# Kernel optimization log

Measured on AMD Instinct MI355X. Metric: run time of the kernel, lower is better.

The kernel has to match this reference:

```python
import jax, jax.numpy as jnp
import numpy as np

B, N, E = 128, 196, 2048   # batch, num_features (14x14), encoder_dim
D, A = 512, 512            # decoder_dim, attention_dim


def setup_inputs() -> dict:
    key = jax.random.key(0)
    ks = jax.random.split(key, 8)
    s_e = 1.0 / np.sqrt(E)
    s_d = 1.0 / np.sqrt(D)
    s_a = 1.0 / np.sqrt(A)
    return {
        "encoder_out": jax.random.normal(ks[0], (B, N, E), dtype=jnp.float32),
        "decoder_hidden": jax.random.normal(ks[1], (B, D), dtype=jnp.float32),
        "We": jax.random.uniform(ks[2], (E, A), jnp.float32, -s_e, s_e),
        "be": jax.random.uniform(ks[3], (A,), jnp.float32, -s_e, s_e),
        "Wd": jax.random.uniform(ks[4], (D, A), jnp.float32, -s_d, s_d),
        "bd": jax.random.uniform(ks[5], (A,), jnp.float32, -s_d, s_d),
        "Wf": jax.random.uniform(ks[6], (A, 1), jnp.float32, -s_a, s_a),
        "bf": jax.random.uniform(ks[7], (1,), jnp.float32, -s_a, s_a),
    }


def reference(encoder_out, decoder_hidden, We, be, Wd, bd, Wf, bf):
    # att1: [B,N,A] projection of encoder features
    att1 = jnp.einsum('bne,ea->bna', encoder_out, We) + be
    # att2: [B,A] projection of decoder state, broadcast over N
    att2 = decoder_hidden @ Wd + bd
    att = jnp.tanh(att1 + att2[:, None, :])          # [B,N,A]
    scores = jnp.einsum('bna,ao->bno', att, Wf) + bf  # [B,N,1]
    alpha = jax.nn.softmax(scores, axis=1)            # softmax over num_features
    context = jnp.sum(encoder_out * alpha, axis=1)    # [B,E]
    return (context, alpha)
```

## Files before the change

### kernel.cpp

```cpp
#include <hip/hip_runtime.h>
#include <hip/hip_bf16.h>
#include <stdint.h>

#define B_   128
#define N_   196
#define E_   2048
#define D_   512
#define A_   512
#define MTOT (B_ * N_)

typedef short  short8  __attribute__((ext_vector_type(8)));
typedef float  floatx4 __attribute__((ext_vector_type(4)));

__device__ __forceinline__ unsigned short f2bf(float f) {
    union { float f; uint32_t u; } v; v.f = f;
    uint32_t r = v.u + 0x7FFFu + ((v.u >> 16) & 1u);
    return (unsigned short)(r >> 16);
}

__global__ void transcvt_k(const float* __restrict__ We, unsigned short* __restrict__ WeT) {
    __shared__ float tile[32][33];
    const int e0 = blockIdx.x * 32, a0 = blockIdx.y * 32;
    const int t = threadIdx.x, tc = t & 31, tr = t >> 5;
#pragma unroll
    for (int i = 0; i < 4; ++i) {
        int r = tr + i * 8;
        tile[r][tc] = We[(size_t)(e0 + r) * A_ + a0 + tc];
    }
    __syncthreads();
#pragma unroll
    for (int i = 0; i < 4; ++i) {
        int r = tr + i * 8;
        WeT[(size_t)(a0 + r) * E_ + e0 + tc] = f2bf(tile[tc][r]);
    }
}

__launch_bounds__(512)
__global__ void att2_k(const float* __restrict__ dh, const float* __restrict__ Wd,
                       const float* __restrict__ bd, const float* __restrict__ be,
                       float* __restrict__ att2p) {
    const int b = blockIdx.x, t = threadIdx.x;
    __shared__ float sdh[D_];
    sdh[t] = dh[b * D_ + t];
    __syncthreads();
    float acc = 0.f;
#pragma unroll 8
    for (int d = 0; d < D_; ++d) acc += sdh[d] * Wd[(size_t)d * A_ + t];
    att2p[(size_t)b * A_ + t] = acc + bd[t] + be[t];
}

__launch_bounds__(256, 3)
__global__ void score_gemm(const float* __restrict__ enc,
                           const unsigned short* __restrict__ WeT,
                           const float* __restrict__ att2p,
                           const float* __restrict__ Wf,
                           float* __restrict__ scoresP) {
    __shared__ __align__(16) unsigned short sA[64 * 40];
    __shared__ __align__(16) unsigned short sB[256 * 32];
    __shared__ float sPart[4][64];

    const int t   = threadIdx.x;
    const int w   = t >> 6;
    const int l   = t & 63;
    const int l15 = l & 15;
    const int q4  = l >> 4;
    const int row0 = blockIdx.y * 64;
    const int cw0  = blockIdx.x * 256;

    floatx4 acc[4][4] = {};

    const int idx1 = t + 256;
    const int ar0 = t >> 3,    ac0 = (t & 7) * 4;
    const int ar1 = idx1 >> 3, ac1 = (idx1 & 7) * 4;
    const float* encA0 = enc + (size_t)(row0 + ar0) * E_ + ac0;
    const float* encA1 = enc + (size_t)(row0 + ar1) * E_ + ac1;

    const unsigned short* bsrc[4];
    int bdst[4];
#pragma unroll
    for (int j = 0; j < 4; ++j) {
        int s    = (w * 4 + j) * 64 + l;
        int nloc = s >> 2;
        int q    = (s & 3) ^ ((nloc >> 2) & 3);
        bsrc[j]  = WeT + (size_t)(cw0 + nloc) * E_ + q * 8;
        bdst[j]  = (w * 4 + j) * 1024;
    }

    for (int k0 = 0; k0 < E_; k0 += 32) {
#pragma unroll
        for (int j = 0; j < 4; ++j) {
            __builtin_amdgcn_global_load_lds(
                (const __attribute__((address_space(1))) uint32_t*)(bsrc[j] + k0),
                (__attribute__((address_space(3))) uint32_t*)((char*)sB + bdst[j]),
                16, 0, 0);
        }
        float4 v0 = *(const float4*)(encA0 + k0);
        float4 v1 = *(const float4*)(encA1 + k0);
        ushort4 h0 = { f2bf(v0.x), f2bf(v0.y), f2bf(v0.z), f2bf(v0.w) };
        ushort4 h1 = { f2bf(v1.x), f2bf(v1.y), f2bf(v1.z), f2bf(v1.w) };
        *(ushort4*)&sA[ar0 * 40 + ac0] = h0;
        *(ushort4*)&sA[ar1 * 40 + ac1] = h1;
        __syncthreads();

        short8 af[4], bfr[4];
#pragma unroll
        for (int mi = 0; mi < 4; ++mi)
            af[mi] = *(const short8*)&sA[(mi * 16 + l15) * 40 + q4 * 8];
#pragma unroll
        for (int ni = 0; ni < 4; ++ni) {
            int nloc = w * 64 + ni * 16 + l15;
            int slot = nloc * 4 + (q4 ^ ((nloc >> 2) & 3));
            bfr[ni] = *(const short8*)&sB[slot * 8];
        }
#pragma unroll
        for (int mi = 0; mi < 4; ++mi)
#pragma unroll
            for (int ni = 0; ni < 4; ++ni)
                acc[mi][ni] = __builtin_amdgcn_mfma_f32_16x16x32_bf16(
                    af[mi], bfr[ni], acc[mi][ni], 0, 0, 0);
        __syncthreads();
    }

    const int cbase = cw0 + w * 64;
    float wfv[4];
#pragma unroll
    for (int ni = 0; ni < 4; ++ni) wfv[ni] = Wf[cbase + ni * 16 + l15];

#pragma unroll
    for (int mi = 0; mi < 4; ++mi) {
#pragma unroll
        for (int r = 0; r < 4; ++r) {
            const int m    = mi * 16 + q4 * 4 + r;
            const int grow = row0 + m;
            const int bb   = grow / N_;
            const float* a2 = att2p + (size_t)bb * A_ + cbase;
            float s = 0.f;
#pragma unroll
            for (int ni = 0; ni < 4; ++ni) {
                float v  = acc[mi][ni][r] + a2[ni * 16 + l15];
                float e  = __expf(2.f * v);
                float th = 1.f - 2.f / (e + 1.f);
                s += th * wfv[ni];
            }
            s += __shfl_xor(s, 1);
            s += __shfl_xor(s, 2);
            s += __shfl_xor(s, 4);
            s += __shfl_xor(s, 8);
            if (l15 == 0) sPart[w][m] = s;
        }
    }
    __syncthreads();
    if (t < 64) {
        float v = sPart[0][t] + sPart[1][t] + sPart[2][t] + sPart[3][t];
        scoresP[(size_t)blockIdx.x * MTOT + row0 + t] = v;
    }
}

__global__ void softmax_k(const float* __restrict__ sp, float* __restrict__ alpha) {
    const int b = blockIdx.x, t = threadIdx.x;
    const int w = t >> 6, l = t & 63;
    __shared__ float red[8];
    float v = -3.0e38f;
    if (t < N_) v = sp[b * N_ + t] + sp[MTOT + b * N_ + t];
    float m = v;
#pragma unroll
    for (int off = 32; off >= 1; off >>= 1) m = fmaxf(m, __shfl_xor(m, off));
    if (l == 0) red[w] = m;
    __syncthreads();
    m = fmaxf(fmaxf(red[0], red[1]), fmaxf(red[2], red[3]));
    float e = 0.f;
    if (t < N_) e = __expf(v - m);
    float s = e;
#pragma unroll
    for (int off = 32; off >= 1; off >>= 1) s += __shfl_xor(s, off);
    if (l == 0) red[4 + w] = s;
    __syncthreads();
    s = red[4] + red[5] + red[6] + red[7];
    if (t < N_) alpha[b * N_ + t] = e / s;
}

__launch_bounds__(256)
__global__ void context_k(const float* __restrict__ enc, const float* __restrict__ alpha,
                          float* __restrict__ ctx) {
    const int chunk = blockIdx.x, b = blockIdx.y;
    const int t = threadIdx.x, tn = t >> 6, tc = t & 63;
    __shared__ float  sAl[N_];
    __shared__ float4 sRed[256];
    if (t < N_) sAl[t] = alpha[b * N_ + t];
    __syncthreads();
    const float* base = enc + (size_t)b * N_ * E_ + chunk * 256 + tc * 4;
    float4 a = make_float4(0.f, 0.f, 0.f, 0.f);
#pragma unroll 7
    for (int n = tn; n < N_; n += 4) {
        float  al = sAl[n];
        float4 v  = *(const float4*)(base + (size_t)n * E_);
        a.x += al * v.x; a.y += al * v.y; a.z += al * v.z; a.w += al * v.w;
    }
    sRed[t] = a;
    __syncthreads();
    if (t < 64) {
        float4 r0 = sRed[t], r1 = sRed[t + 64], r2 = sRed[t + 128], r3 = sRed[t + 192];
        float4 o = make_float4(r0.x + r1.x + r2.x + r3.x, r0.y + r1.y + r2.y + r3.y,
                               r0.z + r1.z + r2.z + r3.z, r0.w + r1.w + r2.w + r3.w);
        *(float4*)(ctx + (size_t)b * E_ + chunk * 256 + t * 4) = o;
    }
}

extern "C" void kernel_launch(void* const* d_in, const int* in_sizes, int n_in,
                              void* d_out, int out_size, void* d_ws, size_t ws_size,
                              hipStream_t stream) {
    const float* enc = (const float*)d_in[0];
    const float* dh  = (const float*)d_in[1];
    const float* We  = (const float*)d_in[2];
    const float* be  = (const float*)d_in[3];
    const float* Wd  = (const float*)d_in[4];
    const float* bd  = (const float*)d_in[5];
    const float* Wf  = (const float*)d_in[6];

    float* out   = (float*)d_out;
    float* ctx   = out;
    float* alpha = out + B_ * E_;

    char* ws = (char*)d_ws;
    unsigned short* WeT  = (unsigned short*)ws;
    float* att2p         = (float*)(ws + (2u << 20));
    float* scoresP       = (float*)(ws + (2u << 20) + (256u << 10));

    transcvt_k <<<dim3(E_ / 32, A_ / 32), 256, 0, stream>>>(We, WeT);
    att2_k     <<<dim3(B_),              512, 0, stream>>>(dh, Wd, bd, be, att2p);
    score_gemm <<<dim3(2, MTOT / 64),    256, 0, stream>>>(enc, WeT, att2p, Wf, scoresP);
    softmax_k  <<<dim3(B_),              256, 0, stream>>>(scoresP, alpha);
    context_k  <<<dim3(E_ / 256, B_),    256, 0, stream>>>(enc, alpha, ctx);
}
```

Baseline: 460.9 us.

## Double-buffer encoder tile in LDS and read WeT fragments directly from global

Restructures the score GEMM main loop. The A tile (encoder rows converted to bf16) is double-buffered in LDS with register prefetch two K-steps ahead, which cuts the barriers to one per K-step. The B operand (WeT) no longer goes through LDS; each wave loads its MFMA fragments straight from global/L2. This frees LDS and overlaps loads with MFMAs, but B fragment loads now depend on cache hits and latency hiding, and there is no reuse of B across waves.

```diff
diff --git a/kernel.cpp b/kernel.cpp
--- a/kernel.cpp
+++ b/kernel.cpp
@@ -55,8 +55,7 @@
                            const float* __restrict__ att2p,
                            const float* __restrict__ Wf,
                            float* __restrict__ scoresP) {
-    __shared__ __align__(16) unsigned short sA[64 * 40];
-    __shared__ __align__(16) unsigned short sB[256 * 32];
+    __shared__ __align__(16) unsigned short sA[2][64 * 32];
     __shared__ float sPart[4][64];
 
     const int t   = threadIdx.x;
@@ -69,59 +68,101 @@
 
     floatx4 acc[4][4] = {};
 
-    const int idx1 = t + 256;
-    const int ar0 = t >> 3,    ac0 = (t & 7) * 4;
-    const int ar1 = idx1 >> 3, ac1 = (idx1 & 7) * 4;
-    const float* encA0 = enc + (size_t)(row0 + ar0) * E_ + ac0;
-    const float* encA1 = enc + (size_t)(row0 + ar1) * E_ + ac1;
-
-    const unsigned short* bsrc[4];
-    int bdst[4];
-#pragma unroll
-    for (int j = 0; j < 4; ++j) {
-        int s    = (w * 4 + j) * 64 + l;
-        int nloc = s >> 2;
-        int q    = (s & 3) ^ ((nloc >> 2) & 3);
-        bsrc[j]  = WeT + (size_t)(cw0 + nloc) * E_ + q * 8;
-        bdst[j]  = (w * 4 + j) * 1024;
-    }
-
-    for (int k0 = 0; k0 < E_; k0 += 32) {
-#pragma unroll
-        for (int j = 0; j < 4; ++j) {
-            __builtin_amdgcn_global_load_lds(
-                (const __attribute__((address_space(1))) uint32_t*)(bsrc[j] + k0),
-                (__attribute__((address_space(3))) uint32_t*)((char*)sB + bdst[j]),
-                16, 0, 0);
-        }
-        float4 v0 = *(const float4*)(encA0 + k0);
-        float4 v1 = *(const float4*)(encA1 + k0);
-        ushort4 h0 = { f2bf(v0.x), f2bf(v0.y), f2bf(v0.z), f2bf(v0.w) };
-        ushort4 h1 = { f2bf(v1.x), f2bf(v1.y), f2bf(v1.z), f2bf(v1.w) };
-        *(ushort4*)&sA[ar0 * 40 + ac0] = h0;
-        *(ushort4*)&sA[ar1 * 40 + ac1] = h1;
+    const int ar = t >> 3;
+    const int ak = (t & 7) * 4;
+    const float* encA0 = enc + (size_t)(row0 + ar) * E_ + ak;
+    const float* encA1 = enc + (size_t)(row0 + ar + 32) * E_ + ak;
+
+    const int qk   = (t & 7) >> 1;
+    const int half = (t & 7) & 1;
+    const int offW0 = ((ar * 4 + (qk ^ ((ar >> 1) & 3))) * 16) + half * 8;
+    const int offW1 = offW0 + 2048;
+
+    const int offR = (l15 * 4 + (q4 ^ ((l15 >> 1) & 3))) * 16;
+
+    const int cbase = cw0 + w * 64;
+    const unsigned short* bp0 = WeT + (size_t)(cbase +  0 + l15) * E_ + q4 * 8;
+    const unsigned short* bp1 = WeT + (size_t)(cbase + 16 + l15) * E_ + q4 * 8;
+    const unsigned short* bp2 = WeT + (size_t)(cbase + 32 + l15) * E_ + q4 * 8;
+    const unsigned short* bp3 = WeT + (size_t)(cbase + 48 + l15) * E_ + q4 * 8;
+
+    float4 X0 = *(const float4*)(encA0);
+    float4 X1 = *(const float4*)(encA1);
+    float4 Y0 = *(const float4*)(encA0 + 32);
+    float4 Y1 = *(const float4*)(encA1 + 32);
+
+    {
+        ushort4 h0 = { f2bf(X0.x), f2bf(X0.y), f2bf(X0.z), f2bf(X0.w) };
+        ushort4 h1 = { f2bf(X1.x), f2bf(X1.y), f2bf(X1.z), f2bf(X1.w) };
+        *(ushort4*)((char*)sA[0] + offW0) = h0;
+        *(ushort4*)((char*)sA[0] + offW1) = h1;
+    }
+    __syncthreads();
+
+    for (int kk = 0; kk < 32; ++kk) {
+        const int  k0      = kk * 2;
+        const bool notlast = (kk < 31);
+
+        if (notlast) {
+            X0 = *(const float4*)(encA0 + (k0 + 2) * 32);
+            X1 = *(const float4*)(encA1 + (k0 + 2) * 32);
+        }
+        {
+            short8 bf0 = *(const short8*)(bp0 + k0 * 32);
+            short8 bf1 = *(const short8*)(bp1 + k0 * 32);
+            short8 bf2 = *(const short8*)(bp2 + k0 * 32);
+            short8 bf3 = *(const short8*)(bp3 + k0 * 32);
+            short8 af[4];
+#pragma unroll
+            for (int mi = 0; mi < 4; ++mi)
+                af[mi] = *(const short8*)((const char*)sA[0] + offR + mi * 1024);
+#pragma unroll
+            for (int mi = 0; mi < 4; ++mi) {
+                acc[mi][0] = __builtin_amdgcn_mfma_f32_16x16x32_bf16(af[mi], bf0, acc[mi][0], 0, 0, 0);
+                acc[mi][1] = __builtin_amdgcn_mfma_f32_16x16x32_bf16(af[mi], bf1, acc[mi][1], 0, 0, 0);
+                acc[mi][2] = __builtin_amdgcn_mfma_f32_16x16x32_bf16(af[mi], bf2, acc[mi][2], 0, 0, 0);
+                acc[mi][3] = __builtin_amdgcn_mfma_f32_16x16x32_bf16(af[mi], bf3, acc[mi][3], 0, 0, 0);
+            }
+        }
+        {
+            ushort4 h0 = { f2bf(Y0.x), f2bf(Y0.y), f2bf(Y0.z), f2bf(Y0.w) };
+            ushort4 h1 = { f2bf(Y1.x), f2bf(Y1.y), f2bf(Y1.z), f2bf(Y1.w) };
+            *(ushort4*)((char*)sA[1] + offW0) = h0;
+            *(ushort4*)((char*)sA[1] + offW1) = h1;
+        }
         __syncthreads();
 
-        short8 af[4], bfr[4];
-#pragma unroll
-        for (int mi = 0; mi < 4; ++mi)
-            af[mi] = *(const short8*)&sA[(mi * 16 + l15) * 40 + q4 * 8];
-#pragma unroll
-        for (int ni = 0; ni < 4; ++ni) {
-            int nloc = w * 64 + ni * 16 + l15;
-            int slot = nloc * 4 + (q4 ^ ((nloc >> 2) & 3));
-            bfr[ni] = *(const short8*)&sB[slot * 8];
-        }
-#pragma unroll
-        for (int mi = 0; mi < 4; ++mi)
-#pragma unroll
-            for (int ni = 0; ni < 4; ++ni)
-                acc[mi][ni] = __builtin_amdgcn_mfma_f32_16x16x32_bf16(
-                    af[mi], bfr[ni], acc[mi][ni], 0, 0, 0);
-        __syncthreads();
-    }
-
-    const int cbase = cw0 + w * 64;
+        const int k1 = k0 + 1;
+        if (notlast) {
+            Y0 = *(const float4*)(encA0 + (k1 + 2) * 32);
+            Y1 = *(const float4*)(encA1 + (k1 + 2) * 32);
+        }
+        {
+            short8 bf0 = *(const short8*)(bp0 + k1 * 32);
+            short8 bf1 = *(const short8*)(bp1 + k1 * 32);
+            short8 bf2 = *(const short8*)(bp2 + k1 * 32);
+            short8 bf3 = *(const short8*)(bp3 + k1 * 32);
+            short8 af[4];
+#pragma unroll
+            for (int mi = 0; mi < 4; ++mi)
+                af[mi] = *(const short8*)((const char*)sA[1] + offR + mi * 1024);
+#pragma unroll
+            for (int mi = 0; mi < 4; ++mi) {
+                acc[mi][0] = __builtin_amdgcn_mfma_f32_16x16x32_bf16(af[mi], bf0, acc[mi][0], 0, 0, 0);
+                acc[mi][1] = __builtin_amdgcn_mfma_f32_16x16x32_bf16(af[mi], bf1, acc[mi][1], 0, 0, 0);
+                acc[mi][2] = __builtin_amdgcn_mfma_f32_16x16x32_bf16(af[mi], bf2, acc[mi][2], 0, 0, 0);
+                acc[mi][3] = __builtin_amdgcn_mfma_f32_16x16x32_bf16(af[mi], bf3, acc[mi][3], 0, 0, 0);
+            }
+        }
+        if (notlast) {
+            ushort4 h0 = { f2bf(X0.x), f2bf(X0.y), f2bf(X0.z), f2bf(X0.w) };
+            ushort4 h1 = { f2bf(X1.x), f2bf(X1.y), f2bf(X1.z), f2bf(X1.w) };
+            *(ushort4*)((char*)sA[0] + offW0) = h0;
+            *(ushort4*)((char*)sA[0] + offW1) = h1;
+            __syncthreads();
+        }
+    }
+
     float wfv[4];
 #pragma unroll
     for (int ni = 0; ni < 4; ++ni) wfv[ni] = Wf[cbase + ni * 16 + l15];
```

After: 511.1 us. +10.9%, slower.

## Load GEMM fragments directly from global into registers with double-buffered prefetch

Applied to the files above, without the earlier changes.

Removes the LDS staging and the per-step block barriers in the score GEMM. Each wave now loads its A (fp32 encoder) and B (bf16 WeT) MFMA fragments straight from global memory into registers, with a two-stage register prefetch. The fp32-to-bf16 pack switches to a cheaper round-half-up perm-based conversion. In exchange there is no data sharing across waves: every wave re-reads the same A rows and the loads are less coalesced. Register pressure also rises, so the launch bound drops to 2 blocks per SM.

```diff
diff --git a/kernel.cpp b/kernel.cpp
--- a/kernel.cpp
+++ b/kernel.cpp
@@ -16,6 +16,12 @@
     union { float f; uint32_t u; } v; v.f = f;
     uint32_t r = v.u + 0x7FFFu + ((v.u >> 16) & 1u);
     return (unsigned short)(r >> 16);
+}
+
+__device__ __forceinline__ uint32_t pkbf(float a, float b) {
+    uint32_t ua = __float_as_uint(a) + 0x8000u;
+    uint32_t ub = __float_as_uint(b) + 0x8000u;
+    return __builtin_amdgcn_perm(ub, ua, 0x07060302u);
 }
 
 __global__ void transcvt_k(const float* __restrict__ We, unsigned short* __restrict__ WeT) {
@@ -49,14 +55,12 @@
     att2p[(size_t)b * A_ + t] = acc + bd[t] + be[t];
 }
 
-__launch_bounds__(256, 3)
+__launch_bounds__(256, 2)
 __global__ void score_gemm(const float* __restrict__ enc,
                            const unsigned short* __restrict__ WeT,
                            const float* __restrict__ att2p,
                            const float* __restrict__ Wf,
                            float* __restrict__ scoresP) {
-    __shared__ __align__(16) unsigned short sA[64 * 40];
-    __shared__ __align__(16) unsigned short sB[256 * 32];
     __shared__ float sPart[4][64];
 
     const int t   = threadIdx.x;
@@ -64,64 +68,71 @@
     const int l   = t & 63;
     const int l15 = l & 15;
     const int q4  = l >> 4;
-    const int row0 = blockIdx.y * 64;
-    const int cw0  = blockIdx.x * 256;
+    const int row0  = blockIdx.y * 64;
+    const int cw0   = blockIdx.x * 256;
+    const int cbase = cw0 + w * 64;
 
     floatx4 acc[4][4] = {};
 
-    const int idx1 = t + 256;
-    const int ar0 = t >> 3,    ac0 = (t & 7) * 4;
-    const int ar1 = idx1 >> 3, ac1 = (idx1 & 7) * 4;
-    const float* encA0 = enc + (size_t)(row0 + ar0) * E_ + ac0;
-    const float* encA1 = enc + (size_t)(row0 + ar1) * E_ + ac1;
-
-    const unsigned short* bsrc[4];
-    int bdst[4];
-#pragma unroll
-    for (int j = 0; j < 4; ++j) {
-        int s    = (w * 4 + j) * 64 + l;
-        int nloc = s >> 2;
-        int q    = (s & 3) ^ ((nloc >> 2) & 3);
-        bsrc[j]  = WeT + (size_t)(cw0 + nloc) * E_ + q * 8;
-        bdst[j]  = (w * 4 + j) * 1024;
-    }
-
-    for (int k0 = 0; k0 < E_; k0 += 32) {
-#pragma unroll
-        for (int j = 0; j < 4; ++j) {
-            __builtin_amdgcn_global_load_lds(
-                (const __attribute__((address_space(1))) uint32_t*)(bsrc[j] + k0),
-                (__attribute__((address_space(3))) uint32_t*)((char*)sB + bdst[j]),
-                16, 0, 0);
-        }
-        float4 v0 = *(const float4*)(encA0 + k0);
-        float4 v1 = *(const float4*)(encA1 + k0);
-        ushort4 h0 = { f2bf(v0.x), f2bf(v0.y), f2bf(v0.z), f2bf(v0.w) };
-        ushort4 h1 = { f2bf(v1.x), f2bf(v1.y), f2bf(v1.z), f2bf(v1.w) };
-        *(ushort4*)&sA[ar0 * 40 + ac0] = h0;
-        *(ushort4*)&sA[ar1 * 40 + ac1] = h1;
-        __syncthreads();
-
-        short8 af[4], bfr[4];
-#pragma unroll
-        for (int mi = 0; mi < 4; ++mi)
-            af[mi] = *(const short8*)&sA[(mi * 16 + l15) * 40 + q4 * 8];
-#pragma unroll
-        for (int ni = 0; ni < 4; ++ni) {
-            int nloc = w * 64 + ni * 16 + l15;
-            int slot = nloc * 4 + (q4 ^ ((nloc >> 2) & 3));
-            bfr[ni] = *(const short8*)&sB[slot * 8];
-        }
-#pragma unroll
-        for (int mi = 0; mi < 4; ++mi)
-#pragma unroll
-            for (int ni = 0; ni < 4; ++ni)
-                acc[mi][ni] = __builtin_amdgcn_mfma_f32_16x16x32_bf16(
-                    af[mi], bfr[ni], acc[mi][ni], 0, 0, 0);
-        __syncthreads();
-    }
-
-    const int cbase = cw0 + w * 64;
+    const float* pa[4];
+    const unsigned short* pb[4];
+#pragma unroll
+    for (int mi = 0; mi < 4; ++mi)
+        pa[mi] = enc + (size_t)(row0 + mi * 16 + l15) * E_ + q4 * 8;
+#pragma unroll
+    for (int ni = 0; ni < 4; ++ni)
+        pb[ni] = WeT + (size_t)(cbase + ni * 16 + l15) * E_ + q4 * 8;
+
+    float4 Afp[2][8];
+    short8 Bst[2][4];
+
+#define LA(s, kk) do { int _ko = (kk) * 32;                                   \
+        _Pragma("unroll")                                                     \
+        for (int mi = 0; mi < 4; ++mi) {                                      \
+            Afp[s][2*mi]   = *(const float4*)(pa[mi] + _ko);                  \
+            Afp[s][2*mi+1] = *(const float4*)(pa[mi] + _ko + 4);              \
+        } } while (0)
+#define LB(s, kk) do { int _ko = (kk) * 32;                                   \
+        _Pragma("unroll")                                                     \
+        for (int ni = 0; ni < 4; ++ni)                                        \
+            Bst[s][ni] = *(const short8*)(pb[ni] + _ko);                      \
+        } while (0)
+
+#define STEP(p, kk, PF) do {                                                  \
+        union { uint32_t u[4]; short8 s; } afu[4];                            \
+        _Pragma("unroll")                                                     \
+        for (int mi = 0; mi < 4; ++mi) {                                      \
+            float4 lo = Afp[p][2*mi], hi = Afp[p][2*mi+1];                    \
+            afu[mi].u[0] = pkbf(lo.x, lo.y);                                  \
+            afu[mi].u[1] = pkbf(lo.z, lo.w);                                  \
+            afu[mi].u[2] = pkbf(hi.x, hi.y);                                  \
+            afu[mi].u[3] = pkbf(hi.z, hi.w);                                  \
+        }                                                                     \
+        if (PF) LA(p, (kk) + 2);                                              \
+        _Pragma("unroll")                                                     \
+        for (int mi = 0; mi < 4; ++mi) {                                      \
+            acc[mi][0] = __builtin_amdgcn_mfma_f32_16x16x32_bf16(afu[mi].s, Bst[p][0], acc[mi][0], 0, 0, 0); \
+            acc[mi][1] = __builtin_amdgcn_mfma_f32_16x16x32_bf16(afu[mi].s, Bst[p][1], acc[mi][1], 0, 0, 0); \
+            acc[mi][2] = __builtin_amdgcn_mfma_f32_16x16x32_bf16(afu[mi].s, Bst[p][2], acc[mi][2], 0, 0, 0); \
+            acc[mi][3] = __builtin_amdgcn_mfma_f32_16x16x32_bf16(afu[mi].s, Bst[p][3], acc[mi][3], 0, 0, 0); \
+        }                                                                     \
+        if (PF) LB(p, (kk) + 2);                                              \
+    } while (0)
+
+    LA(0, 0); LB(0, 0);
+    LA(1, 1); LB(1, 1);
+
+    for (int kk = 0; kk < 62; kk += 2) {
+        STEP(0, kk, true);
+        STEP(1, kk + 1, true);
+    }
+    STEP(0, 62, false);
+    STEP(1, 63, false);
+
+#undef LA
+#undef LB
+#undef STEP
+
     float wfv[4];
 #pragma unroll
     for (int ni = 0; ni < 4; ++ni) wfv[ni] = Wf[cbase + ni * 16 + l15];
```

After: 639.4 us. +38.7%, slower.

## Retile score GEMM to 128x128 with async fp32 A loads and in-register bf16 pack

Applied to the files above, without the earlier changes.

The score GEMM moves from 64x256 tiles to 128x128 tiles on a 2x2 wave grid, so the softmax now sums four partial score slices instead of two. Encoder fp32 data is now copied straight into LDS with global_load_lds using an XOR swizzle, then converted to bf16 in registers with a cheaper pack that rounds by adding 0x8000 instead of round-to-nearest-even. This removes the register round-trip and manual conversion stores on the A side, but it doubles the LDS bytes per A element and repeats the conversion in every wave that reads a row.

```diff
diff --git a/kernel.cpp b/kernel.cpp
--- a/kernel.cpp
+++ b/kernel.cpp
@@ -16,6 +16,12 @@
     union { float f; uint32_t u; } v; v.f = f;
     uint32_t r = v.u + 0x7FFFu + ((v.u >> 16) & 1u);
     return (unsigned short)(r >> 16);
+}
+
+__device__ __forceinline__ uint32_t pkbf(float a, float b) {
+    uint32_t ua = __float_as_uint(a) + 0x8000u;
+    uint32_t ub = __float_as_uint(b) + 0x8000u;
+    return __builtin_amdgcn_perm(ub, ua, 0x07060302u);
 }
 
 __global__ void transcvt_k(const float* __restrict__ We, unsigned short* __restrict__ WeT) {
@@ -55,8 +61,7 @@
                            const float* __restrict__ att2p,
                            const float* __restrict__ Wf,
                            float* __restrict__ scoresP) {
-    __shared__ __align__(16) unsigned short sA[64 * 40];
-    __shared__ __align__(16) unsigned short sB[256 * 32];
+    __shared__ __align__(16) char sMem[16384 + 8192];
     __shared__ float sPart[4][64];
 
     const int t   = threadIdx.x;
@@ -64,64 +69,86 @@
     const int l   = t & 63;
     const int l15 = l & 15;
     const int q4  = l >> 4;
-    const int row0 = blockIdx.y * 64;
-    const int cw0  = blockIdx.x * 256;
+    const int wm  = w >> 1;
+    const int wn  = w & 1;
+    const int row0 = blockIdx.y * 128;
+    const int col0 = blockIdx.x * 128;
 
     floatx4 acc[4][4] = {};
 
-    const int idx1 = t + 256;
-    const int ar0 = t >> 3,    ac0 = (t & 7) * 4;
-    const int ar1 = idx1 >> 3, ac1 = (idx1 & 7) * 4;
-    const float* encA0 = enc + (size_t)(row0 + ar0) * E_ + ac0;
-    const float* encA1 = enc + (size_t)(row0 + ar1) * E_ + ac1;
-
-    const unsigned short* bsrc[4];
-    int bdst[4];
+    const float* aSrc[4];
+    int aDst[4];
 #pragma unroll
     for (int j = 0; j < 4; ++j) {
-        int s    = (w * 4 + j) * 64 + l;
-        int nloc = s >> 2;
-        int q    = (s & 3) ^ ((nloc >> 2) & 3);
-        bsrc[j]  = WeT + (size_t)(cw0 + nloc) * E_ + q * 8;
-        bdst[j]  = (w * 4 + j) * 1024;
-    }
-
-    for (int k0 = 0; k0 < E_; k0 += 32) {
-#pragma unroll
-        for (int j = 0; j < 4; ++j) {
+        int s  = w * 256 + j * 64 + l;
+        int r  = s >> 3, p = s & 7;
+        int cs = p ^ (r & 7);
+        aSrc[j] = enc + (size_t)(row0 + r) * E_ + cs * 4;
+        aDst[j] = (w * 256 + j * 64) * 16;
+    }
+    const unsigned short* bSrc[2];
+    int bDst[2];
+#pragma unroll
+    for (int j = 0; j < 2; ++j) {
+        int s  = w * 128 + j * 64 + l;
+        int n  = s >> 2, p = s & 3;
+        int cs = p ^ ((n >> 2) & 3);
+        bSrc[j] = WeT + (size_t)(col0 + n) * E_ + cs * 8;
+        bDst[j] = 16384 + (w * 128 + j * 64) * 16;
+    }
+
+    const int p0 = (2 * q4) ^ (l15 & 7);
+    int offA[4], offA2[4], offB[4];
+#pragma unroll
+    for (int mi = 0; mi < 4; ++mi) {
+        int rA  = wm * 64 + mi * 16 + l15;
+        offA[mi]  = rA * 128 + p0 * 16;
+        offA2[mi] = rA * 128 + (p0 ^ 1) * 16;
+    }
+#pragma unroll
+    for (int ni = 0; ni < 4; ++ni) {
+        int nB = wn * 64 + ni * 16 + l15;
+        offB[ni] = 16384 + nB * 64 + (q4 ^ ((l15 >> 2) & 3)) * 16;
+    }
+
+    for (int kk = 0; kk < 64; ++kk) {
+#pragma unroll
+        for (int j = 0; j < 4; ++j)
             __builtin_amdgcn_global_load_lds(
-                (const __attribute__((address_space(1))) uint32_t*)(bsrc[j] + k0),
-                (__attribute__((address_space(3))) uint32_t*)((char*)sB + bdst[j]),
-                16, 0, 0);
+                (const __attribute__((address_space(1))) uint32_t*)(aSrc[j] + kk * 32),
+                (__attribute__((address_space(3))) uint32_t*)(sMem + aDst[j]), 16, 0, 0);
+#pragma unroll
+        for (int j = 0; j < 2; ++j)
+            __builtin_amdgcn_global_load_lds(
+                (const __attribute__((address_space(1))) uint32_t*)(bSrc[j] + kk * 32),
+                (__attribute__((address_space(3))) uint32_t*)(sMem + bDst[j]), 16, 0, 0);
+        __syncthreads();
+
+        short8 bfr[4];
+        union { uint32_t u[4]; short8 s; } af[4];
+#pragma unroll
+        for (int ni = 0; ni < 4; ++ni)
+            bfr[ni] = *(const short8*)(sMem + offB[ni]);
+#pragma unroll
+        for (int mi = 0; mi < 4; ++mi) {
+            float4 lo = *(const float4*)(sMem + offA[mi]);
+            float4 hi = *(const float4*)(sMem + offA2[mi]);
+            af[mi].u[0] = pkbf(lo.x, lo.y);
+            af[mi].u[1] = pkbf(lo.z, lo.w);
+            af[mi].u[2] = pkbf(hi.x, hi.y);
+            af[mi].u[3] = pkbf(hi.z, hi.w);
         }
-        float4 v0 = *(const float4*)(encA0 + k0);
-        float4 v1 = *(const float4*)(encA1 + k0);
-        ushort4 h0 = { f2bf(v0.x), f2bf(v0.y), f2bf(v0.z), f2bf(v0.w) };
-        ushort4 h1 = { f2bf(v1.x), f2bf(v1.y), f2bf(v1.z), f2bf(v1.w) };
-        *(ushort4*)&sA[ar0 * 40 + ac0] = h0;
-        *(ushort4*)&sA[ar1 * 40 + ac1] = h1;
+#pragma unroll
+        for (int mi = 0; mi < 4; ++mi) {
+            acc[mi][0] = __builtin_amdgcn_mfma_f32_16x16x32_bf16(af[mi].s, bfr[0], acc[mi][0], 0, 0, 0);
+            acc[mi][1] = __builtin_amdgcn_mfma_f32_16x16x32_bf16(af[mi].s, bfr[1], acc[mi][1], 0, 0, 0);
+            acc[mi][2] = __builtin_amdgcn_mfma_f32_16x16x32_bf16(af[mi].s, bfr[2], acc[mi][2], 0, 0, 0);
+            acc[mi][3] = __builtin_amdgcn_mfma_f32_16x16x32_bf16(af[mi].s, bfr[3], acc[mi][3], 0, 0, 0);
+        }
         __syncthreads();
-
-        short8 af[4], bfr[4];
-#pragma unroll
-        for (int mi = 0; mi < 4; ++mi)
-            af[mi] = *(const short8*)&sA[(mi * 16 + l15) * 40 + q4 * 8];
-#pragma unroll
-        for (int ni = 0; ni < 4; ++ni) {
-            int nloc = w * 64 + ni * 16 + l15;
-            int slot = nloc * 4 + (q4 ^ ((nloc >> 2) & 3));
-            bfr[ni] = *(const short8*)&sB[slot * 8];
-        }
-#pragma unroll
-        for (int mi = 0; mi < 4; ++mi)
-#pragma unroll
-            for (int ni = 0; ni < 4; ++ni)
-                acc[mi][ni] = __builtin_amdgcn_mfma_f32_16x16x32_bf16(
-                    af[mi], bfr[ni], acc[mi][ni], 0, 0, 0);
-        __syncthreads();
-    }
-
-    const int cbase = cw0 + w * 64;
+    }
+
+    const int cbase = col0 + wn * 64;
     float wfv[4];
 #pragma unroll
     for (int ni = 0; ni < 4; ++ni) wfv[ni] = Wf[cbase + ni * 16 + l15];
@@ -131,7 +158,7 @@
 #pragma unroll
         for (int r = 0; r < 4; ++r) {
             const int m    = mi * 16 + q4 * 4 + r;
-            const int grow = row0 + m;
+            const int grow = row0 + wm * 64 + m;
             const int bb   = grow / N_;
             const float* a2 = att2p + (size_t)bb * A_ + cbase;
             float s = 0.f;
@@ -150,8 +177,9 @@
         }
     }
     __syncthreads();
-    if (t < 64) {
-        float v = sPart[0][t] + sPart[1][t] + sPart[2][t] + sPart[3][t];
+    if (t < 128) {
+        const int h = t >> 6, m = t & 63;
+        float v = sPart[h * 2 + 0][m] + sPart[h * 2 + 1][m];
         scoresP[(size_t)blockIdx.x * MTOT + row0 + t] = v;
     }
 }
@@ -161,7 +189,8 @@
     const int w = t >> 6, l = t & 63;
     __shared__ float red[8];
     float v = -3.0e38f;
-    if (t < N_) v = sp[b * N_ + t] + sp[MTOT + b * N_ + t];
+    if (t < N_) v = sp[b * N_ + t] + sp[MTOT + b * N_ + t]
+                  + sp[2 * MTOT + b * N_ + t] + sp[3 * MTOT + b * N_ + t];
     float m = v;
 #pragma unroll
     for (int off = 32; off >= 1; off >>= 1) m = fmaxf(m, __shfl_xor(m, off));
@@ -228,7 +257,7 @@
 
     transcvt_k <<<dim3(E_ / 32, A_ / 32), 256, 0, stream>>>(We, WeT);
     att2_k     <<<dim3(B_),              512, 0, stream>>>(dh, Wd, bd, be, att2p);
-    score_gemm <<<dim3(2, MTOT / 64),    256, 0, stream>>>(enc, WeT, att2p, Wf, scoresP);
+    score_gemm <<<dim3(4, MTOT / 128),   256, 0, stream>>>(enc, WeT, att2p, Wf, scoresP);
     softmax_k  <<<dim3(B_),              256, 0, stream>>>(scoresP, alpha);
     context_k  <<<dim3(E_ / 256, B_),    256, 0, stream>>>(enc, alpha, ctx);
 }
```

After: 495.6 us. 1.08x slower.
